# Optimization experiments

Measured on AMD Instinct MI355X. Metric: run time of the kernel, lower is better.

Reference implementation:

```python
import jax, jax.numpy as jnp
import numpy as np

BETA = 0.92
THRESHOLD = 1.0
SLOPE = 25.0  # snntorch surrogate.fast_sigmoid default slope


@jax.custom_vjp
def spike_fn(x):
    # Heaviside forward, fast-sigmoid surrogate backward
    return (x > 0).astype(x.dtype)


def _spike_fwd(x):
    return (x > 0).astype(x.dtype), x


def _spike_bwd(x, g):
    return (g / (SLOPE * jnp.abs(x) + 1.0) ** 2,)


spike_fn.defvjp(_spike_fwd, _spike_bwd)


def _lif(cur, mem_prev):
    # snntorch Leaky (reset_mechanism='subtract'): reset is based on the
    # PREVIOUS membrane and is detached from the graph.
    reset = jax.lax.stop_gradient((mem_prev > THRESHOLD).astype(cur.dtype))
    mem = BETA * mem_prev + cur - reset * THRESHOLD
    spk = spike_fn(mem - THRESHOLD)
    return spk, mem


def setup_inputs() -> dict:
    key = jax.random.key(0)
    ks = jax.random.split(key, 7)
    T, B, D_IN, H = 100, 4096, 9, 96
    return {
        "spike_input": (jax.random.uniform(ks[0], (T, B, D_IN)) < 0.3).astype(jnp.float32),
        "W1": jax.random.normal(ks[1], (H, D_IN), jnp.float32) * (1.0 / np.sqrt(D_IN)),
        "b1": jax.random.normal(ks[2], (H,), jnp.float32) * 0.01,
        "W2": jax.random.normal(ks[3], (H, H), jnp.float32) * (1.0 / np.sqrt(H)),
        "b2": jax.random.normal(ks[4], (H,), jnp.float32) * 0.01,
        "W3": jax.random.normal(ks[5], (H // 2, H), jnp.float32) * (1.0 / np.sqrt(H)),
        "b3": jax.random.normal(ks[6], (H // 2,), jnp.float32) * 0.01,
    }


def reference(spike_input, W1, b1, W2, b2, W3, b3):
    # spike_input: [T, B, input_dim]
    B = spike_input.shape[1]
    H = W1.shape[0]
    H3 = W3.shape[0]
    dt = spike_input.dtype
    init = (jnp.zeros((B, H), dt), jnp.zeros((B, H), dt), jnp.zeros((B, H3), dt))

    def step(carry, x_t):
        m1, m2, m3 = carry
        s1, m1 = _lif(x_t @ W1.T + b1, m1)
        s2, m2 = _lif(s1 @ W2.T + b2, m2)
        s3, m3 = _lif(s2 @ W3.T + b3, m3)
        return (m1, m2, m3), (s3, m3)

    _, (spk_rec, mem_rec) = jax.lax.scan(step, init, spike_input)
    # [T, B, hidden//2] each (fc_out is never applied in the original forward)
    return spk_rec, mem_rec
```

## Files before the change

### kernel.cpp

```cpp
#include <hip/hip_runtime.h>


constexpr int T_STEPS = 100;
constexpr int BATCH   = 4096;
constexpr int D_INP   = 9;
constexpr int H       = 96;
constexpr int H3      = 48;
constexpr int WAVES   = 8;
constexpr int BPW     = 2;
constexpr int NB      = WAVES * BPW;
constexpr int BLOCK   = WAVES * 64;
constexpr int NBLK    = BATCH / NB;
constexpr int TC      = 2;

__device__ __forceinline__ float lif_step(float sum, float bias, float& m) {
    const float cur   = __fadd_rn(sum, bias);
    const float mp    = m;
    const float reset = (mp > 1.0f) ? 1.0f : 0.0f;
    const float mn    = __fsub_rn(__fadd_rn(__fmul_rn(0.92f, mp), cur), reset);
    m = mn;
    return mn;
}

#if defined(__has_builtin)
#if __has_builtin(__builtin_amdgcn_mov_dpp)
#define SNN_HAS_DPP 1
#endif
#endif

template <int CTRL>
__device__ __forceinline__ float xadd(float c) {
#ifdef SNN_HAS_DPP
    const int o = __builtin_amdgcn_mov_dpp(__float_as_int(c), CTRL, 0xF, 0xF, false);
    return __fadd_rn(c, __int_as_float(o));
#else
    return __fadd_rn(c, __shfl_xor(c, (CTRL == 0xB1) ? 1 : 2, 64));
#endif
}

__device__ __forceinline__ float quad_red(float c) {
    return xadd<0x4E>(xadd<0xB1>(c));
}

#define UNPACK2S(dw, row, sfarr)                                              \
    sfarr[row][0]     = (float)( (dw)        & 255u);                         \
    sfarr[row][1]     = (float)(((dw) >> 8)  & 255u);                         \
    sfarr[(row)+1][0] = (float)(((dw) >> 16) & 255u);                         \
    sfarr[(row)+1][1] = (float)( (dw) >> 24);

#define FMA8S(accv, wv, sfarr, base)                                          \
    accv[0] = fmaf(wv.x, sfarr[(base)+0][0], accv[0]);                        \
    accv[1] = fmaf(wv.x, sfarr[(base)+0][1], accv[1]);                        \
    accv[0] = fmaf(wv.y, sfarr[(base)+1][0], accv[0]);                        \
    accv[1] = fmaf(wv.y, sfarr[(base)+1][1], accv[1]);                        \
    accv[0] = fmaf(wv.z, sfarr[(base)+2][0], accv[0]);                        \
    accv[1] = fmaf(wv.z, sfarr[(base)+2][1], accv[1]);                        \
    accv[0] = fmaf(wv.w, sfarr[(base)+3][0], accv[0]);                        \
    accv[1] = fmaf(wv.w, sfarr[(base)+3][1], accv[1]);

#define FENCE_LGKM() asm volatile("s_waitcnt lgkmcnt(0)" ::: "memory")

__global__ __launch_bounds__(BLOCK, 2)
void snn_tc2(const float* __restrict__ x,
             const float* __restrict__ W1g, const float* __restrict__ b1g,
             const float* __restrict__ W2g, const float* __restrict__ b2g,
             const float* __restrict__ W3g, const float* __restrict__ b3g,
             float* __restrict__ out)
{
    __shared__ __align__(16) float          W2L[36 * 64 * 4];
    __shared__ __align__(16) float          W3L[18 * 64 * 4];
    __shared__ __align__(16) float          W1L[96 * 12];
    __shared__ __align__(16) unsigned short spk[TC][WAVES][4][24];

    const int tid = threadIdx.x;
    const int w   = tid >> 6;
    const int l   = tid & 63;
    const int q   = l >> 2;
    const int r   = l & 3;
    const int r01 = r & 1;
    const int bL  = l >> 5;
    const int bg0 = blockIdx.x * NB + w * BPW;

    for (int idx = tid; idx < 36 * 64; idx += BLOCK) {
        const int c = idx >> 6, ll = idx & 63;
        const int s = c / 6, jq = c % 6, qq = ll >> 2, rr = ll & 3;
        #pragma unroll
        for (int jj = 0; jj < 4; ++jj)
            W2L[idx * 4 + jj] = W2g[(16 * s + qq) * H + 16 * jq + 4 * jj + rr];
    }
    for (int idx = tid; idx < 18 * 64; idx += BLOCK) {
        const int c = idx >> 6, ll = idx & 63;
        const int s = c / 6, jq = c % 6, qq = ll >> 2, rr = ll & 3;
        #pragma unroll
        for (int jj = 0; jj < 4; ++jj)
            W3L[idx * 4 + jj] = W3g[(16 * s + qq) * H + 16 * jq + 4 * jj + rr];
    }
    for (int idx = tid; idx < 96 * 12; idx += BLOCK) {
        const int n = idx / 12, k = idx % 12;
        W1L[idx] = (k < 9) ? W1g[n * D_INP + k] : 0.0f;
    }

    float bb1[3], bb2[6], bb3[3];
    #pragma unroll
    for (int i = 0; i < 3; ++i) bb1[i] = b1g[(l & 31) + 32 * i];
    #pragma unroll
    for (int s = 0; s < 6; ++s) bb2[s] = b2g[16 * s + q];
    #pragma unroll
    for (int s = 0; s < 3; ++s) bb3[s] = b3g[16 * s + q];
    float m1[3] = {}, m2[6] = {}, m3[3] = {};

    float* out_spk = out;
    float* out_mem = out + (size_t)T_STEPS * BATCH * H3;

    __syncthreads();

    #pragma unroll 1
    for (int tc = 0; tc < T_STEPS; tc += TC) {
        float xr[TC][D_INP];
        const float* xp = x + ((size_t)tc * BATCH + bg0 + bL) * D_INP;
        #pragma unroll
        for (int tp = 0; tp < TC; ++tp) {
            #pragma unroll
            for (int k = 0; k < D_INP; ++k)
                xr[tp][k] = xp[(size_t)tp * BATCH * D_INP + k];
        }

        #pragma unroll
        for (int tp = 0; tp < TC; ++tp) {
            unsigned char* s1b = (unsigned char*)&spk[tp][w][0][0];
            #pragma unroll
            for (int i = 0; i < 3; ++i) {
                const int n1 = (l & 31) + 32 * i;
                const float4 wa = *(const float4*)&W1L[n1 * 12];
                const float4 wb = *(const float4*)&W1L[n1 * 12 + 4];
                const float  w8 = W1L[n1 * 12 + 8];
                const float q0 = __fmul_rn(wa.x, xr[tp][0]);
                const float q1 = __fmul_rn(wa.y, xr[tp][1]);
                const float q2 = __fmul_rn(wa.z, xr[tp][2]);
                const float q3 = __fmul_rn(wa.w, xr[tp][3]);
                const float q4 = __fmul_rn(wb.x, xr[tp][4]);
                const float q5 = __fmul_rn(wb.y, xr[tp][5]);
                const float q6 = __fmul_rn(wb.z, xr[tp][6]);
                const float q7 = __fmul_rn(wb.w, xr[tp][7]);
                const float q8 = __fmul_rn(w8,   xr[tp][8]);
                const float r0 = __fadd_rn(__fadd_rn(q8, q0), q4);
                const float r1 = __fadd_rn(q1, q5);
                const float r2 = __fadd_rn(q2, q6);
                const float r3 = __fadd_rn(q3, q7);
                const float s  = __fadd_rn(__fadd_rn(r0, r1), __fadd_rn(r2, r3));
                const float mn = lif_step(s, bb1[i], m1[i]);
                s1b[((n1 & 3) * 24 + (n1 >> 2)) * 2 + bL] =
                    (mn > 1.0f) ? (unsigned char)1 : (unsigned char)0;
            }
        }
        FENCE_LGKM();

        float acc[TC][6][2] = {};
        #pragma unroll
        for (int jc = 0; jc < 3; ++jc) {
            const uint4 sp0 = *(const uint4*)&spk[0][w][r][8 * jc];
            const uint4 sp1 = *(const uint4*)&spk[1][w][r][8 * jc];
            float sf0[8][2], sf1[8][2];
            UNPACK2S(sp0.x, 0, sf0) UNPACK2S(sp0.y, 2, sf0)
            UNPACK2S(sp0.z, 4, sf0) UNPACK2S(sp0.w, 6, sf0)
            UNPACK2S(sp1.x, 0, sf1) UNPACK2S(sp1.y, 2, sf1)
            UNPACK2S(sp1.z, 4, sf1) UNPACK2S(sp1.w, 6, sf1)
            #pragma unroll
            for (int sh = 0; sh < 2; ++sh) {
                float4 wA[3], wB[3];
                #pragma unroll
                for (int si = 0; si < 3; ++si) {
                    const int s = 3 * sh + si;
                    wA[si] = *(const float4*)&W2L[((s * 6 + 2 * jc)     * 64 + l) * 4];
                    wB[si] = *(const float4*)&W2L[((s * 6 + 2 * jc + 1) * 64 + l) * 4];
                }
                #pragma unroll
                for (int si = 0; si < 3; ++si) {
                    FMA8S(acc[0][3 * sh + si], wA[si], sf0, 0)
                    FMA8S(acc[0][3 * sh + si], wB[si], sf0, 4)
                    FMA8S(acc[1][3 * sh + si], wA[si], sf1, 0)
                    FMA8S(acc[1][3 * sh + si], wB[si], sf1, 4)
                }
            }
        }
        FENCE_LGKM();

        #pragma unroll
        for (int tp = 0; tp < TC; ++tp) {
            unsigned char* s2b = (unsigned char*)&spk[tp][w][0][0];
            #pragma unroll
            for (int s = 0; s < 6; ++s) {
                const float g0 = quad_red(acc[tp][s][0]);
                const float g1 = quad_red(acc[tp][s][1]);
                const float sv = r01 ? g1 : g0;
                const float mn = lif_step(sv, bb2[s], m2[s]);
                if (r < 2) {
                    const int n2 = 16 * s + q;
                    s2b[((n2 & 3) * 24 + (n2 >> 2)) * 2 + r] =
                        (mn > 1.0f) ? (unsigned char)1 : (unsigned char)0;
                }
            }
        }
        FENCE_LGKM();

        float a3[TC][3][2] = {};
        #pragma unroll
        for (int jc = 0; jc < 3; ++jc) {
            const uint4 sp0 = *(const uint4*)&spk[0][w][r][8 * jc];
            const uint4 sp1 = *(const uint4*)&spk[1][w][r][8 * jc];
            float sf0[8][2], sf1[8][2];
            UNPACK2S(sp0.x, 0, sf0) UNPACK2S(sp0.y, 2, sf0)
            UNPACK2S(sp0.z, 4, sf0) UNPACK2S(sp0.w, 6, sf0)
            UNPACK2S(sp1.x, 0, sf1) UNPACK2S(sp1.y, 2, sf1)
            UNPACK2S(sp1.z, 4, sf1) UNPACK2S(sp1.w, 6, sf1)
            float4 wA[3], wB[3];
            #pragma unroll
            for (int s = 0; s < 3; ++s) {
                wA[s] = *(const float4*)&W3L[((s * 6 + 2 * jc)     * 64 + l) * 4];
                wB[s] = *(const float4*)&W3L[((s * 6 + 2 * jc + 1) * 64 + l) * 4];
            }
            #pragma unroll
            for (int s = 0; s < 3; ++s) {
                FMA8S(a3[0][s], wA[s], sf0, 0)
                FMA8S(a3[0][s], wB[s], sf0, 4)
                FMA8S(a3[1][s], wA[s], sf1, 0)
                FMA8S(a3[1][s], wB[s], sf1, 4)
            }
        }

        #pragma unroll
        for (int tp = 0; tp < TC; ++tp) {
            #pragma unroll
            for (int s = 0; s < 3; ++s) {
                const float g0 = quad_red(a3[tp][s][0]);
                const float g1 = quad_red(a3[tp][s][1]);
                const float sv = r01 ? g1 : g0;
                const float mn = lif_step(sv, bb3[s], m3[s]);
                if (r < 2) {
                    const size_t ob =
                        ((size_t)(tc + tp) * BATCH + bg0 + r) * H3 + 16 * s + q;
                    out_spk[ob] = (mn > 1.0f) ? 1.0f : 0.0f;
                    out_mem[ob] = mn;
                }
            }
        }
        FENCE_LGKM();
    }
}

extern "C" void kernel_launch(void* const* d_in, const int* in_sizes, int n_in,
                              void* d_out, int out_size, void* d_ws, size_t ws_size,
                              hipStream_t stream)
{
    const float* x  = (const float*)d_in[0];
    const float* W1 = (const float*)d_in[1];
    const float* b1 = (const float*)d_in[2];
    const float* W2 = (const float*)d_in[3];
    const float* b2 = (const float*)d_in[4];
    const float* W3 = (const float*)d_in[5];
    const float* b3 = (const float*)d_in[6];
    float* out = (float*)d_out;

    snn_tc2<<<dim3(NBLK), dim3(BLOCK), 0, stream>>>(
        x, W1, b1, W2, b2, W3, b3, out);
}
```

Before: 402.2 us.

## Process four timesteps per chunk and split layer-2 into two output halves

Raises the per-chunk timestep count from 2 to 4, so each W2/W3 fragment loaded from LDS is reused across four spike vectors. Layer 2 is computed in two halves of three output slices each, and the resulting spikes are packed into a bitmask before being written back to LDS. This keeps accumulator register pressure bounded. W1 storage is split into separate float4 arrays. The cost is more registers and more LDS for spike buffers, which may hurt occupancy under the launch bounds of 2 blocks per SM.

```diff
diff --git a/kernel.cpp b/kernel.cpp
--- a/kernel.cpp
+++ b/kernel.cpp
@@ -11,7 +11,7 @@
 constexpr int NB      = WAVES * BPW;
 constexpr int BLOCK   = WAVES * 64;
 constexpr int NBLK    = BATCH / NB;
-constexpr int TC      = 2;
+constexpr int TC      = 4;
 
 __device__ __forceinline__ float lif_step(float sum, float bias, float& m) {
     const float cur   = __fadd_rn(sum, bias);
@@ -61,15 +61,17 @@
 #define FENCE_LGKM() asm volatile("s_waitcnt lgkmcnt(0)" ::: "memory")
 
 __global__ __launch_bounds__(BLOCK, 2)
-void snn_tc2(const float* __restrict__ x,
-             const float* __restrict__ W1g, const float* __restrict__ b1g,
-             const float* __restrict__ W2g, const float* __restrict__ b2g,
-             const float* __restrict__ W3g, const float* __restrict__ b3g,
-             float* __restrict__ out)
+void snn_t4(const float* __restrict__ x,
+            const float* __restrict__ W1g, const float* __restrict__ b1g,
+            const float* __restrict__ W2g, const float* __restrict__ b2g,
+            const float* __restrict__ W3g, const float* __restrict__ b3g,
+            float* __restrict__ out)
 {
     __shared__ __align__(16) float          W2L[36 * 64 * 4];
     __shared__ __align__(16) float          W3L[18 * 64 * 4];
-    __shared__ __align__(16) float          W1L[96 * 12];
+    __shared__ __align__(16) float4         W1a[96];
+    __shared__ __align__(16) float4         W1b[96];
+    __shared__ __align__(16) float          W1c[96];
     __shared__ __align__(16) unsigned short spk[TC][WAVES][4][24];
 
     const int tid = threadIdx.x;
@@ -95,9 +97,13 @@
         for (int jj = 0; jj < 4; ++jj)
             W3L[idx * 4 + jj] = W3g[(16 * s + qq) * H + 16 * jq + 4 * jj + rr];
     }
-    for (int idx = tid; idx < 96 * 12; idx += BLOCK) {
-        const int n = idx / 12, k = idx % 12;
-        W1L[idx] = (k < 9) ? W1g[n * D_INP + k] : 0.0f;
+    if (tid < 96) {
+        const int n = tid;
+        W1a[n] = make_float4(W1g[n * 9 + 0], W1g[n * 9 + 1],
+                             W1g[n * 9 + 2], W1g[n * 9 + 3]);
+        W1b[n] = make_float4(W1g[n * 9 + 4], W1g[n * 9 + 5],
+                             W1g[n * 9 + 6], W1g[n * 9 + 7]);
+        W1c[n] = W1g[n * 9 + 8];
     }
 
     float bb1[3], bb2[6], bb3[3];
@@ -131,9 +137,9 @@
             #pragma unroll
             for (int i = 0; i < 3; ++i) {
                 const int n1 = (l & 31) + 32 * i;
-                const float4 wa = *(const float4*)&W1L[n1 * 12];
-                const float4 wb = *(const float4*)&W1L[n1 * 12 + 4];
-                const float  w8 = W1L[n1 * 12 + 8];
+                const float4 wa = W1a[n1];
+                const float4 wb = W1b[n1];
+                const float  w8 = W1c[n1];
                 const float q0 = __fmul_rn(wa.x, xr[tp][0]);
                 const float q1 = __fmul_rn(wa.y, xr[tp][1]);
                 const float q2 = __fmul_rn(wa.z, xr[tp][2]);
@@ -155,31 +161,77 @@
         }
         FENCE_LGKM();
 
-        float acc[TC][6][2] = {};
-        #pragma unroll
-        for (int jc = 0; jc < 3; ++jc) {
-            const uint4 sp0 = *(const uint4*)&spk[0][w][r][8 * jc];
-            const uint4 sp1 = *(const uint4*)&spk[1][w][r][8 * jc];
-            float sf0[8][2], sf1[8][2];
-            UNPACK2S(sp0.x, 0, sf0) UNPACK2S(sp0.y, 2, sf0)
-            UNPACK2S(sp0.z, 4, sf0) UNPACK2S(sp0.w, 6, sf0)
-            UNPACK2S(sp1.x, 0, sf1) UNPACK2S(sp1.y, 2, sf1)
-            UNPACK2S(sp1.z, 4, sf1) UNPACK2S(sp1.w, 6, sf1)
-            #pragma unroll
-            for (int sh = 0; sh < 2; ++sh) {
+        unsigned sbits = 0u;
+
+        {
+            float acc[TC][3][2] = {};
+            #pragma unroll
+            for (int jc = 0; jc < 3; ++jc) {
                 float4 wA[3], wB[3];
                 #pragma unroll
                 for (int si = 0; si < 3; ++si) {
-                    const int s = 3 * sh + si;
+                    wA[si] = *(const float4*)&W2L[((si * 6 + 2 * jc)     * 64 + l) * 4];
+                    wB[si] = *(const float4*)&W2L[((si * 6 + 2 * jc + 1) * 64 + l) * 4];
+                }
+                #pragma unroll
+                for (int tp = 0; tp < TC; ++tp) {
+                    const uint4 sp = *(const uint4*)&spk[tp][w][r][8 * jc];
+                    float sf[8][2];
+                    UNPACK2S(sp.x, 0, sf) UNPACK2S(sp.y, 2, sf)
+                    UNPACK2S(sp.z, 4, sf) UNPACK2S(sp.w, 6, sf)
+                    #pragma unroll
+                    for (int si = 0; si < 3; ++si) {
+                        FMA8S(acc[tp][si], wA[si], sf, 0)
+                        FMA8S(acc[tp][si], wB[si], sf, 4)
+                    }
+                }
+            }
+            #pragma unroll
+            for (int tp = 0; tp < TC; ++tp) {
+                #pragma unroll
+                for (int si = 0; si < 3; ++si) {
+                    const float g0 = quad_red(acc[tp][si][0]);
+                    const float g1 = quad_red(acc[tp][si][1]);
+                    const float sv = r01 ? g1 : g0;
+                    const float mn = lif_step(sv, bb2[si], m2[si]);
+                    sbits |= (mn > 1.0f) ? (1u << (tp * 6 + si)) : 0u;
+                }
+            }
+        }
+
+        {
+            float acc[TC][3][2] = {};
+            #pragma unroll
+            for (int jc = 0; jc < 3; ++jc) {
+                float4 wA[3], wB[3];
+                #pragma unroll
+                for (int si = 0; si < 3; ++si) {
+                    const int s = 3 + si;
                     wA[si] = *(const float4*)&W2L[((s * 6 + 2 * jc)     * 64 + l) * 4];
                     wB[si] = *(const float4*)&W2L[((s * 6 + 2 * jc + 1) * 64 + l) * 4];
                 }
                 #pragma unroll
+                for (int tp = 0; tp < TC; ++tp) {
+                    const uint4 sp = *(const uint4*)&spk[tp][w][r][8 * jc];
+                    float sf[8][2];
+                    UNPACK2S(sp.x, 0, sf) UNPACK2S(sp.y, 2, sf)
+                    UNPACK2S(sp.z, 4, sf) UNPACK2S(sp.w, 6, sf)
+                    #pragma unroll
+                    for (int si = 0; si < 3; ++si) {
+                        FMA8S(acc[tp][si], wA[si], sf, 0)
+                        FMA8S(acc[tp][si], wB[si], sf, 4)
+                    }
+                }
+            }
+            #pragma unroll
+            for (int tp = 0; tp < TC; ++tp) {
+                #pragma unroll
                 for (int si = 0; si < 3; ++si) {
-                    FMA8S(acc[0][3 * sh + si], wA[si], sf0, 0)
-                    FMA8S(acc[0][3 * sh + si], wB[si], sf0, 4)
-                    FMA8S(acc[1][3 * sh + si], wA[si], sf1, 0)
-                    FMA8S(acc[1][3 * sh + si], wB[si], sf1, 4)
+                    const float g0 = quad_red(acc[tp][si][0]);
+                    const float g1 = quad_red(acc[tp][si][1]);
+                    const float sv = r01 ? g1 : g0;
+                    const float mn = lif_step(sv, bb2[3 + si], m2[3 + si]);
+                    sbits |= (mn > 1.0f) ? (1u << (tp * 6 + 3 + si)) : 0u;
                 }
             }
         }
@@ -190,14 +242,9 @@
             unsigned char* s2b = (unsigned char*)&spk[tp][w][0][0];
             #pragma unroll
             for (int s = 0; s < 6; ++s) {
-                const float g0 = quad_red(acc[tp][s][0]);
-                const float g1 = quad_red(acc[tp][s][1]);
-                const float sv = r01 ? g1 : g0;
-                const float mn = lif_step(sv, bb2[s], m2[s]);
                 if (r < 2) {
-                    const int n2 = 16 * s + q;
-                    s2b[((n2 & 3) * 24 + (n2 >> 2)) * 2 + r] =
-                        (mn > 1.0f) ? (unsigned char)1 : (unsigned char)0;
+                    s2b[((q & 3) * 24 + 4 * s + (q >> 2)) * 2 + r] =
+                        (unsigned char)((sbits >> (tp * 6 + s)) & 1u);
                 }
             }
         }
@@ -206,13 +253,6 @@
         float a3[TC][3][2] = {};
         #pragma unroll
         for (int jc = 0; jc < 3; ++jc) {
-            const uint4 sp0 = *(const uint4*)&spk[0][w][r][8 * jc];
-            const uint4 sp1 = *(const uint4*)&spk[1][w][r][8 * jc];
-            float sf0[8][2], sf1[8][2];
-            UNPACK2S(sp0.x, 0, sf0) UNPACK2S(sp0.y, 2, sf0)
-            UNPACK2S(sp0.z, 4, sf0) UNPACK2S(sp0.w, 6, sf0)
-            UNPACK2S(sp1.x, 0, sf1) UNPACK2S(sp1.y, 2, sf1)
-            UNPACK2S(sp1.z, 4, sf1) UNPACK2S(sp1.w, 6, sf1)
             float4 wA[3], wB[3];
             #pragma unroll
             for (int s = 0; s < 3; ++s) {
@@ -220,11 +260,16 @@
                 wB[s] = *(const float4*)&W3L[((s * 6 + 2 * jc + 1) * 64 + l) * 4];
             }
             #pragma unroll
-            for (int s = 0; s < 3; ++s) {
-                FMA8S(a3[0][s], wA[s], sf0, 0)
-                FMA8S(a3[0][s], wB[s], sf0, 4)
-                FMA8S(a3[1][s], wA[s], sf1, 0)
-                FMA8S(a3[1][s], wB[s], sf1, 4)
+            for (int tp = 0; tp < TC; ++tp) {
+                const uint4 sp = *(const uint4*)&spk[tp][w][r][8 * jc];
+                float sf[8][2];
+                UNPACK2S(sp.x, 0, sf) UNPACK2S(sp.y, 2, sf)
+                UNPACK2S(sp.z, 4, sf) UNPACK2S(sp.w, 6, sf)
+                #pragma unroll
+                for (int s = 0; s < 3; ++s) {
+                    FMA8S(a3[tp][s], wA[s], sf, 0)
+                    FMA8S(a3[tp][s], wB[s], sf, 4)
+                }
             }
         }
 
@@ -261,6 +306,6 @@
     const float* b3 = (const float*)d_in[6];
     float* out = (float*)d_out;
 
-    snn_tc2<<<dim3(NBLK), dim3(BLOCK), 0, stream>>>(
+    snn_t4<<<dim3(NBLK), dim3(BLOCK), 0, stream>>>(
         x, W1, b1, W2, b2, W3, b3, out);
 }
```

New measurement: 409.5 us. About the same (+1.8%).
